# Kernel optimization log

Hardware: AMD Instinct MI355X
Metric: run time of the kernel (lower is better)

## Reference

```python
import jax, jax.numpy as jnp
import numpy as np

S, H, E, DFF = 8192, 1024, 8, 4096
CAPACITY = (S * 1) // E  # capacity_factor=1.0, k=1 -> 1024 (>= min_capacity 4)


def setup_inputs() -> dict:
    key = jax.random.key(0)
    ks = jax.random.split(key, 6)
    sc_in = 1.0 / np.sqrt(H)
    sc_ff = 1.0 / np.sqrt(DFF)
    return {
        "hidden_states": jax.random.normal(ks[0], (S, H), dtype=jnp.float32),
        "wg": jax.random.normal(ks[1], (H, E), dtype=jnp.float32) * sc_in,
        "w1": jax.random.normal(ks[2], (E, H, DFF), dtype=jnp.float32) * sc_in,
        "b1": jnp.zeros((E, DFF), dtype=jnp.float32),
        "w2": jax.random.normal(ks[3], (E, DFF, H), dtype=jnp.float32) * sc_ff,
        "b2": jnp.zeros((E, H), dtype=jnp.float32),
    }


def _top1_gate(x, wg):
    # DeepSpeed top1gating (noisy_gate_policy=None, used_token=None)
    logits = x @ wg                                   # [S, E]
    gates = jax.nn.softmax(logits, axis=-1)           # [S, E]
    idx = jnp.argmax(gates, axis=-1)                  # [S]
    mask1 = jax.nn.one_hot(idx, E, dtype=gates.dtype) # [S, E]
    # load-balancing aux loss (uses pre-capacity mask)
    me = jnp.mean(gates, axis=0)
    ce = jnp.mean(mask1, axis=0)
    l_aux = jnp.sum(me * ce) * E
    # capacity-based token dropping
    locations1 = jnp.cumsum(mask1, axis=0) - 1.0      # position within expert
    mask1 = mask1 * (locations1 < CAPACITY)
    exp_counts = jnp.sum(mask1, axis=0).astype(jnp.int32)
    loc_s = jnp.sum(locations1 * mask1, axis=1).astype(jnp.int32)   # [S]
    loc_sc = jax.nn.one_hot(loc_s, CAPACITY, dtype=gates.dtype)     # [S, C]
    combine = jnp.einsum("se,sc->sec", gates * mask1, loc_sc)       # [S, E, C]
    dispatch = (combine > 0).astype(gates.dtype)
    return l_aux, combine, dispatch, exp_counts


def reference(hidden_states, wg, w1, b1, w2, b2):
    l_aux, combine, dispatch, exp_counts = _top1_gate(hidden_states, wg)
    # dispatch tokens to expert slots: [E, C, H]
    disp = jnp.einsum("sec,sh->ech", dispatch, hidden_states)
    # grouped expert FFN (GELU MLP)
    h1 = jax.nn.gelu(jnp.einsum("ech,ehf->ecf", disp, w1) + b1[:, None, :])
    eo = jnp.einsum("ecf,efh->ech", h1, w2) + b2[:, None, :]
    # combine back to token order, weighted by gate values
    out = jnp.einsum("sec,ech->sh", combine, eo)      # [S, H]
    # dropout prob = 0.0 -> identity
    return out, l_aux, exp_counts
```

## Files before the change

### kernel.cpp

```cpp
#include <hip/hip_runtime.h>

#define S_TOK 8192
#define H_DIM 1024
#define NE    8
#define CAP   1024
#define DFF   4096

typedef unsigned short u16;
typedef __bf16 bf16_t;
typedef bf16_t bf16x8 __attribute__((ext_vector_type(8)));
typedef float  f32x4  __attribute__((ext_vector_type(4)));

__device__ __forceinline__ u16 f2bf(float f) {
  union { float f; unsigned u; } a; a.f = f;
  unsigned u = a.u;
  u += 0x7fffu + ((u >> 16) & 1u);
  return (u16)(u >> 16);
}

__device__ __forceinline__ float gelu_tanh(float x) {
  const float c = 0.7978845608028654f;
  float t = tanhf(c * (x + 0.044715f * x * x * x));
  return 0.5f * x * (1.0f + t);
}

__global__ void gate_kernel(const float* __restrict__ x, const float* __restrict__ wg,
                            float* __restrict__ gate, int* __restrict__ expert,
                            int* __restrict__ rank, int* __restrict__ blockCnt,
                            float* __restrict__ blockMe) {
  __shared__ float sg[16][8];
  __shared__ int   se[16];
  int tid = threadIdx.x, lane = tid & 63, w = tid >> 6;
  int b = blockIdx.x;
  for (int j = 0; j < 4; ++j) {
    int t = w * 4 + j;
    int s = b * 16 + t;
    const float* xr = x + (size_t)s * H_DIM;
    float acc[8];
#pragma unroll
    for (int e = 0; e < 8; ++e) acc[e] = 0.f;
#pragma unroll
    for (int i = 0; i < 16; ++i) {
      int h = i * 64 + lane;
      float xv = xr[h];
      float4 wa = *(const float4*)(wg + h * 8);
      float4 wb = *(const float4*)(wg + h * 8 + 4);
      acc[0] += xv * wa.x; acc[1] += xv * wa.y; acc[2] += xv * wa.z; acc[3] += xv * wa.w;
      acc[4] += xv * wb.x; acc[5] += xv * wb.y; acc[6] += xv * wb.z; acc[7] += xv * wb.w;
    }
#pragma unroll
    for (int off = 32; off >= 1; off >>= 1)
#pragma unroll
      for (int e = 0; e < 8; ++e) acc[e] += __shfl_down(acc[e], off);
    if (lane == 0) {
      float mx = acc[0];
#pragma unroll
      for (int e = 1; e < 8; ++e) mx = fmaxf(mx, acc[e]);
      float g[8], Z = 0.f;
#pragma unroll
      for (int e = 0; e < 8; ++e) { g[e] = expf(acc[e] - mx); Z += g[e]; }
      int am = 0; float best = acc[0];
#pragma unroll
      for (int e = 1; e < 8; ++e) if (acc[e] > best) { best = acc[e]; am = e; }
      float inv = 1.f / Z;
#pragma unroll
      for (int e = 0; e < 8; ++e) sg[t][e] = g[e] * inv;
      se[t] = am;
      gate[s] = g[am] * inv;
      expert[s] = am;
    }
  }
  __syncthreads();
  if (tid < 16) {
    int e = se[tid], r = 0;
    for (int t2 = 0; t2 < tid; ++t2) r += (se[t2] == e) ? 1 : 0;
    rank[b * 16 + tid] = r;
  }
  if (tid < 8) {
    int c = 0; float m = 0.f;
#pragma unroll
    for (int t = 0; t < 16; ++t) { c += (se[t] == tid) ? 1 : 0; m += sg[t][tid]; }
    blockCnt[b * 8 + tid] = c;
    blockMe[b * 8 + tid] = m;
  }
}

__global__ void scan_kernel(const int* __restrict__ blockCnt, const float* __restrict__ blockMe,
                            int* __restrict__ blockOff, int* __restrict__ counts,
                            float* __restrict__ tail) {
  int tid = threadIdx.x;
  int e = tid >> 6, lane = tid & 63;
  int run = 0; float msum = 0.f;
  for (int c = 0; c < 8; ++c) {
    int b = c * 64 + lane;
    int v = blockCnt[b * 8 + e];
    float mv = blockMe[b * 8 + e];
    int sc = v;
#pragma unroll
    for (int off = 1; off < 64; off <<= 1) {
      int u = __shfl_up(sc, off);
      if (lane >= off) sc += u;
    }
    blockOff[b * 8 + e] = run + sc - v;
    run += __shfl(sc, 63);
#pragma unroll
    for (int off = 32; off >= 1; off >>= 1) mv += __shfl_down(mv, off);
    msum += __shfl(mv, 0);
  }
  __shared__ float sm[8];
  __shared__ int scnt[8];
  if (lane == 0) {
    sm[e] = msum; scnt[e] = run;
    counts[e] = run < CAP ? run : CAP;
  }
  __syncthreads();
  if (tid == 0) {
    float la = 0.f;
    for (int i = 0; i < 8; ++i)
      la += (sm[i] / (float)S_TOK) * ((float)scnt[i] / (float)S_TOK);
    tail[0] = la * (float)NE;
    for (int i = 0; i < 8; ++i) {
      int cc = scnt[i] < CAP ? scnt[i] : CAP;
      tail[1 + i] = (float)cc;
    }
  }
}

__global__ void assign_kernel(const int* __restrict__ expert, const int* __restrict__ rank,
                              const int* __restrict__ blockOff, int* __restrict__ slot_token) {
  int s = blockIdx.x * 256 + threadIdx.x;
  int e = expert[s];
  int pos = blockOff[(s >> 4) * 8 + e] + rank[s];
  if (pos < CAP) slot_token[e * CAP + pos] = s;
}

__global__ void gather_kernel(const float* __restrict__ x, const int* __restrict__ slot_token,
                              const int* __restrict__ counts, u16* __restrict__ disp) {
  int slot = blockIdx.x;
  int e = slot >> 10, c = slot & 1023;
  int t = threadIdx.x;
  ushort4 v4;
  if (c < counts[e]) {
    int s = slot_token[slot];
    float4 v = *(const float4*)(x + (size_t)s * H_DIM + t * 4);
    v4.x = f2bf(v.x); v4.y = f2bf(v.y); v4.z = f2bf(v.z); v4.w = f2bf(v.w);
  } else {
    v4.x = 0; v4.y = 0; v4.z = 0; v4.w = 0;
  }
  *(ushort4*)(disp + (size_t)slot * H_DIM + t * 4) = v4;
}

__global__ void transpose_convert(const float* __restrict__ src0, u16* __restrict__ dst0,
                                  int R, int C) {
  __shared__ float tile[32][33];
  int e = blockIdx.z;
  const float* src = src0 + (size_t)e * R * C;
  u16* dst = dst0 + (size_t)e * R * C;
  int c0 = blockIdx.x * 32, r0 = blockIdx.y * 32;
  int xq = threadIdx.x & 31, yq = threadIdx.x >> 5;
#pragma unroll
  for (int i = 0; i < 32; i += 8)
    tile[yq + i][xq] = src[(size_t)(r0 + yq + i) * C + c0 + xq];
  __syncthreads();
#pragma unroll
  for (int i = 0; i < 32; i += 8)
    dst[(size_t)(c0 + yq + i) * R + r0 + xq] = f2bf(tile[xq][yq + i]);
}

__device__ __forceinline__ void stage_tile(const u16* g, int ldk, u16* lds) {
  int tid = threadIdx.x;
  int lane = tid & 63, w = tid >> 6;
#pragma unroll
  for (int r = 0; r < 2; ++r) {
    int p = (w * 2 + r) * 64 + lane;
    int row = p >> 2;
    int kq = (p & 3) ^ ((row >> 1) & 3);
    const u16* gp = g + (size_t)row * ldk + kq * 8;
    u16* lp = lds + (w * 2 + r) * 512;
    __builtin_amdgcn_global_load_lds((__attribute__((address_space(1))) int*)(gp),
                                     (__attribute__((address_space(3))) int*)(lp),
                                     16, 0, 0);
  }
}

template <int KDIM>
__device__ __forceinline__ void gemm_core(const u16* A, const u16* Bt, int lda, int ldb,
                                          u16* As, u16* Bs, f32x4 acc[4][4]) {
  int tid = threadIdx.x;
  int lane = tid & 63;
  int w = tid >> 6, wm = w >> 1, wn = w & 1;
  int q = lane >> 4, l15 = lane & 15;
  int aoff[4], boff[4];
#pragma unroll
  for (int t = 0; t < 4; ++t) {
    int ra = wm * 64 + t * 16 + l15;
    aoff[t] = ra * 32 + ((q ^ ((ra >> 1) & 3)) * 8);
    int rb = wn * 64 + t * 16 + l15;
    boff[t] = rb * 32 + ((q ^ ((rb >> 1) & 3)) * 8);
  }
  for (int kt = 0; kt < KDIM; kt += 32) {
    stage_tile(A + kt, lda, As);
    stage_tile(Bt + kt, ldb, Bs);
    __syncthreads();
    bf16x8 af[4], bfr[4];
#pragma unroll
    for (int t = 0; t < 4; ++t) af[t] = *(const bf16x8*)(As + aoff[t]);
#pragma unroll
    for (int t = 0; t < 4; ++t) bfr[t] = *(const bf16x8*)(Bs + boff[t]);
#pragma unroll
    for (int mt = 0; mt < 4; ++mt)
#pragma unroll
      for (int nt = 0; nt < 4; ++nt)
        acc[mt][nt] = __builtin_amdgcn_mfma_f32_16x16x32_bf16(af[mt], bfr[nt], acc[mt][nt], 0, 0, 0);
    __syncthreads();
  }
}

__global__ __launch_bounds__(256, 2) void gemm1_kernel(const u16* __restrict__ disp,
                                                       const u16* __restrict__ w1t,
                                                       const float* __restrict__ b1,
                                                       u16* __restrict__ h1) {
  __shared__ __align__(16) u16 As[4096];
  __shared__ __align__(16) u16 Bs[4096];
  int e = blockIdx.z;
  int m0 = blockIdx.y * 128, n0 = blockIdx.x * 128;
  const u16* A  = disp + (size_t)e * CAP * H_DIM + (size_t)m0 * H_DIM;
  const u16* Bt = w1t + (size_t)e * DFF * H_DIM + (size_t)n0 * H_DIM;
  f32x4 acc[4][4];
  f32x4 zero = {0.f, 0.f, 0.f, 0.f};
#pragma unroll
  for (int i = 0; i < 4; ++i)
#pragma unroll
    for (int j = 0; j < 4; ++j) acc[i][j] = zero;
  gemm_core<H_DIM>(A, Bt, H_DIM, H_DIM, As, Bs, acc);
  int tid = threadIdx.x, lane = tid & 63, w = tid >> 6, wm = w >> 1, wn = w & 1;
  int q = lane >> 4, l15 = lane & 15;
  const float* b1e = b1 + e * DFF;
  u16* out = h1 + (size_t)e * CAP * DFF;
#pragma unroll
  for (int mt = 0; mt < 4; ++mt)
#pragma unroll
    for (int nt = 0; nt < 4; ++nt) {
      int col = n0 + wn * 64 + nt * 16 + l15;
      float bias = b1e[col];
#pragma unroll
      for (int r = 0; r < 4; ++r) {
        int row = m0 + wm * 64 + mt * 16 + q * 4 + r;
        out[(size_t)row * DFF + col] = f2bf(gelu_tanh(acc[mt][nt][r] + bias));
      }
    }
}

__global__ __launch_bounds__(256, 2) void gemm2_kernel(const u16* __restrict__ h1,
                                                       const u16* __restrict__ w2t,
                                                       const float* __restrict__ b2,
                                                       const int* __restrict__ slot_token,
                                                       const float* __restrict__ gate,
                                                       const int* __restrict__ counts,
                                                       float* __restrict__ out) {
  __shared__ __align__(16) u16 As[4096];
  __shared__ __align__(16) u16 Bs[4096];
  int e = blockIdx.z;
  int m0 = blockIdx.y * 128, n0 = blockIdx.x * 128;
  const u16* A  = h1 + (size_t)e * CAP * DFF + (size_t)m0 * DFF;
  const u16* Bt = w2t + (size_t)e * H_DIM * DFF + (size_t)n0 * DFF;
  f32x4 acc[4][4];
  f32x4 zero = {0.f, 0.f, 0.f, 0.f};
#pragma unroll
  for (int i = 0; i < 4; ++i)
#pragma unroll
    for (int j = 0; j < 4; ++j) acc[i][j] = zero;
  gemm_core<DFF>(A, Bt, DFF, DFF, As, Bs, acc);
  int tid = threadIdx.x, lane = tid & 63, w = tid >> 6, wm = w >> 1, wn = w & 1;
  int q = lane >> 4, l15 = lane & 15;
  int cnt = counts[e];
  const float* b2e = b2 + e * H_DIM;
#pragma unroll
  for (int mt = 0; mt < 4; ++mt) {
    int tok[4]; float gv[4];
#pragma unroll
    for (int r = 0; r < 4; ++r) {
      int c = m0 + wm * 64 + mt * 16 + q * 4 + r;
      if (c < cnt) { int s = slot_token[e * CAP + c]; tok[r] = s; gv[r] = gate[s]; }
      else { tok[r] = -1; gv[r] = 0.f; }
    }
#pragma unroll
    for (int nt = 0; nt < 4; ++nt) {
      int col = n0 + wn * 64 + nt * 16 + l15;
      float bias = b2e[col];
#pragma unroll
      for (int r = 0; r < 4; ++r)
        if (tok[r] >= 0)
          out[(size_t)tok[r] * H_DIM + col] = gv[r] * (acc[mt][nt][r] + bias);
    }
  }
}

extern "C" void kernel_launch(void* const* d_in, const int* in_sizes, int n_in,
                              void* d_out, int out_size, void* d_ws, size_t ws_size,
                              hipStream_t stream) {
  const float* x  = (const float*)d_in[0];
  const float* wg = (const float*)d_in[1];
  const float* w1 = (const float*)d_in[2];
  const float* b1 = (const float*)d_in[3];
  const float* w2 = (const float*)d_in[4];
  const float* b2 = (const float*)d_in[5];
  float* out = (float*)d_out;
  char* ws = (char*)d_ws;
  const size_t MB = 1024 * 1024;
  u16* w1t  = (u16*)(ws);
  u16* w2t  = (u16*)(ws + 64 * MB);
  u16* disp = (u16*)(ws + 128 * MB);
  u16* h1   = (u16*)(ws + 144 * MB);
  char* sm = ws + 208 * MB;
  float* gate      = (float*)(sm);
  int*   expert    = (int*)(sm + 32 * 1024);
  int*   rank      = (int*)(sm + 64 * 1024);
  int*   slot_tok  = (int*)(sm + 96 * 1024);
  int*   blockCnt  = (int*)(sm + 128 * 1024);
  int*   blockOff  = (int*)(sm + 144 * 1024);
  float* blockMe   = (float*)(sm + 160 * 1024);
  int*   counts    = (int*)(sm + 176 * 1024);

  hipMemsetAsync(d_out, 0, (size_t)out_size * sizeof(float), stream);
  gate_kernel<<<512, 256, 0, stream>>>(x, wg, gate, expert, rank, blockCnt, blockMe);
  scan_kernel<<<1, 512, 0, stream>>>(blockCnt, blockMe, blockOff, counts,
                                     out + (size_t)S_TOK * H_DIM);
  assign_kernel<<<32, 256, 0, stream>>>(expert, rank, blockOff, slot_tok);
  gather_kernel<<<8192, 256, 0, stream>>>(x, slot_tok, counts, disp);
  transpose_convert<<<dim3(DFF / 32, H_DIM / 32, NE), 256, 0, stream>>>(w1, w1t, H_DIM, DFF);
  transpose_convert<<<dim3(H_DIM / 32, DFF / 32, NE), 256, 0, stream>>>(w2, w2t, DFF, H_DIM);
  gemm1_kernel<<<dim3(DFF / 128, CAP / 128, NE), 256, 0, stream>>>(disp, w1t, b1, h1);
  gemm2_kernel<<<dim3(H_DIM / 128, CAP / 128, NE), 256, 0, stream>>>(h1, w2t, b2,
                                                                     slot_tok, gate, counts, out);
}
```

Measured before the change: 631.0 us.

## Widen weight transpose to 64x64 vector tiles and give gemm2 eight waves

The weight transpose/convert kernel now works on 64x64 tiles with float4 loads and ushort4 bf16 stores instead of scalar 32x32 accesses, to cut memory transaction count. gemm2 now runs 512 threads per block with eight waves: half stage A and half stage B into LDS, and each wave computes a 64x32 sub-tile. This raises wave parallelism for the small 256-block grid. The new gemm2 inner loop is single-buffered with two barriers per k-step, so latency hiding rests on occupancy rather than prefetching.

```diff
diff --git a/kernel.cpp b/kernel.cpp
--- a/kernel.cpp
+++ b/kernel.cpp
@@ -152,19 +152,32 @@
 
 __global__ void transpose_convert(const float* __restrict__ src0, u16* __restrict__ dst0,
                                   int R, int C) {
-  __shared__ float tile[32][33];
+  __shared__ float tile[64][65];
   int e = blockIdx.z;
   const float* src = src0 + (size_t)e * R * C;
   u16* dst = dst0 + (size_t)e * R * C;
-  int c0 = blockIdx.x * 32, r0 = blockIdx.y * 32;
-  int xq = threadIdx.x & 31, yq = threadIdx.x >> 5;
-#pragma unroll
-  for (int i = 0; i < 32; i += 8)
-    tile[yq + i][xq] = src[(size_t)(r0 + yq + i) * C + c0 + xq];
+  int c0 = blockIdx.x * 64, r0 = blockIdx.y * 64;
+  int g = threadIdx.x & 15, rr = threadIdx.x >> 4;
+#pragma unroll
+  for (int p = 0; p < 4; ++p) {
+    int r = rr + p * 16;
+    float4 v = *(const float4*)(src + (size_t)(r0 + r) * C + c0 + g * 4);
+    tile[r][g * 4 + 0] = v.x;
+    tile[r][g * 4 + 1] = v.y;
+    tile[r][g * 4 + 2] = v.z;
+    tile[r][g * 4 + 3] = v.w;
+  }
   __syncthreads();
 #pragma unroll
-  for (int i = 0; i < 32; i += 8)
-    dst[(size_t)(c0 + yq + i) * R + r0 + xq] = f2bf(tile[xq][yq + i]);
+  for (int p = 0; p < 4; ++p) {
+    int c = rr + p * 16;
+    ushort4 o;
+    o.x = f2bf(tile[g * 4 + 0][c]);
+    o.y = f2bf(tile[g * 4 + 1][c]);
+    o.z = f2bf(tile[g * 4 + 2][c]);
+    o.w = f2bf(tile[g * 4 + 3][c]);
+    *(ushort4*)(dst + (size_t)(c0 + c) * R + r0 + g * 4) = o;
+  }
 }
 
 __device__ __forceinline__ void stage_tile(const u16* g, int ldk, u16* lds) {
@@ -251,7 +264,7 @@
     }
 }
 
-__global__ __launch_bounds__(256, 2) void gemm2_kernel(const u16* __restrict__ h1,
+__global__ __launch_bounds__(512, 4) void gemm2_kernel(const u16* __restrict__ h1,
                                                        const u16* __restrict__ w2t,
                                                        const float* __restrict__ b2,
                                                        const int* __restrict__ slot_token,
@@ -264,15 +277,59 @@
   int m0 = blockIdx.y * 128, n0 = blockIdx.x * 128;
   const u16* A  = h1 + (size_t)e * CAP * DFF + (size_t)m0 * DFF;
   const u16* Bt = w2t + (size_t)e * H_DIM * DFF + (size_t)n0 * DFF;
-  f32x4 acc[4][4];
+  int tid = threadIdx.x, lane = tid & 63, w = tid >> 6;
+  int wm = w >> 2, wn = w & 3;
+  int q = lane >> 4, l15 = lane & 15;
+  f32x4 acc[4][2];
   f32x4 zero = {0.f, 0.f, 0.f, 0.f};
 #pragma unroll
-  for (int i = 0; i < 4; ++i)
-#pragma unroll
-    for (int j = 0; j < 4; ++j) acc[i][j] = zero;
-  gemm_core<DFF>(A, Bt, DFF, DFF, As, Bs, acc);
-  int tid = threadIdx.x, lane = tid & 63, w = tid >> 6, wm = w >> 1, wn = w & 1;
-  int q = lane >> 4, l15 = lane & 15;
+  for (int i = 0; i < 4; ++i) { acc[i][0] = zero; acc[i][1] = zero; }
+
+  const u16* gsrc = (w < 4) ? A : Bt;
+  u16* ldst = (w < 4) ? As : Bs;
+  int q4 = w & 3;
+  const u16* gp0[2]; u16* lp[2];
+#pragma unroll
+  for (int r = 0; r < 2; ++r) {
+    int p = (q4 * 2 + r) * 64 + lane;
+    int srow = p >> 2;
+    int skq = (p & 3) ^ ((srow >> 1) & 3);
+    gp0[r] = gsrc + (size_t)srow * DFF + skq * 8;
+    lp[r] = ldst + (q4 * 2 + r) * 512;
+  }
+
+  int aoff[4], boff[2];
+#pragma unroll
+  for (int t = 0; t < 4; ++t) {
+    int ra = wm * 64 + t * 16 + l15;
+    aoff[t] = ra * 32 + ((q ^ ((ra >> 1) & 3)) * 8);
+  }
+#pragma unroll
+  for (int t = 0; t < 2; ++t) {
+    int rb = wn * 32 + t * 16 + l15;
+    boff[t] = rb * 32 + ((q ^ ((rb >> 1) & 3)) * 8);
+  }
+
+  for (int kt = 0; kt < DFF; kt += 32) {
+#pragma unroll
+    for (int r = 0; r < 2; ++r)
+      __builtin_amdgcn_global_load_lds((__attribute__((address_space(1))) int*)(gp0[r] + kt),
+                                       (__attribute__((address_space(3))) int*)(lp[r]),
+                                       16, 0, 0);
+    __syncthreads();
+    bf16x8 af[4], bfr[2];
+#pragma unroll
+    for (int t = 0; t < 4; ++t) af[t] = *(const bf16x8*)(As + aoff[t]);
+#pragma unroll
+    for (int t = 0; t < 2; ++t) bfr[t] = *(const bf16x8*)(Bs + boff[t]);
+#pragma unroll
+    for (int mt = 0; mt < 4; ++mt)
+#pragma unroll
+      for (int nt = 0; nt < 2; ++nt)
+        acc[mt][nt] = __builtin_amdgcn_mfma_f32_16x16x32_bf16(af[mt], bfr[nt], acc[mt][nt], 0, 0, 0);
+    __syncthreads();
+  }
+
   int cnt = counts[e];
   const float* b2e = b2 + e * H_DIM;
 #pragma unroll
@@ -285,8 +342,8 @@
       else { tok[r] = -1; gv[r] = 0.f; }
     }
 #pragma unroll
-    for (int nt = 0; nt < 4; ++nt) {
-      int col = n0 + wn * 64 + nt * 16 + l15;
+    for (int nt = 0; nt < 2; ++nt) {
+      int col = n0 + wn * 32 + nt * 16 + l15;
       float bias = b2e[col];
 #pragma unroll
       for (int r = 0; r < 4; ++r)
@@ -328,9 +385,9 @@
                                      out + (size_t)S_TOK * H_DIM);
   assign_kernel<<<32, 256, 0, stream>>>(expert, rank, blockOff, slot_tok);
   gather_kernel<<<8192, 256, 0, stream>>>(x, slot_tok, counts, disp);
-  transpose_convert<<<dim3(DFF / 32, H_DIM / 32, NE), 256, 0, stream>>>(w1, w1t, H_DIM, DFF);
-  transpose_convert<<<dim3(H_DIM / 32, DFF / 32, NE), 256, 0, stream>>>(w2, w2t, DFF, H_DIM);
+  transpose_convert<<<dim3(DFF / 64, H_DIM / 64, NE), 256, 0, stream>>>(w1, w1t, H_DIM, DFF);
+  transpose_convert<<<dim3(H_DIM / 64, DFF / 64, NE), 256, 0, stream>>>(w2, w2t, DFF, H_DIM);
   gemm1_kernel<<<dim3(DFF / 128, CAP / 128, NE), 256, 0, stream>>>(disp, w1t, b1, h1);
-  gemm2_kernel<<<dim3(H_DIM / 128, CAP / 128, NE), 256, 0, stream>>>(h1, w2t, b2,
+  gemm2_kernel<<<dim3(H_DIM / 128, CAP / 128, NE), 512, 0, stream>>>(h1, w2t, b2,
                                                                      slot_tok, gate, counts, out);
 }
```

Measured after the change: 616.5 us. 2.3% less time.

## Fuse fp32 weight conversion into GEMM B-tile staging and split-K gemm2

Applied to the files above, without the earlier changes.

Drops the two transpose_convert passes over the fp32 expert weights. Each GEMM now reads w1/w2 in fp32 directly, converts to bf16 in registers and writes a padded LDS tile. gemm2 is split into two K-halves that write fp32 partials, and a new combine kernel sums them, adds bias, applies the gate and scatters to token order. This removes a full read/write pass over about 256MB of weights and raises gemm2 parallelism. In exchange, every M-tile block re-reads and re-converts fp32 weights (8x redundant), B loads are no longer asynchronous LDS loads, and the partials add extra traffic.

```diff
diff --git a/kernel.cpp b/kernel.cpp
--- a/kernel.cpp
+++ b/kernel.cpp
@@ -10,6 +10,8 @@
 typedef __bf16 bf16_t;
 typedef bf16_t bf16x8 __attribute__((ext_vector_type(8)));
 typedef float  f32x4  __attribute__((ext_vector_type(4)));
+
+#define BSTRIDE 40
 
 __device__ __forceinline__ u16 f2bf(float f) {
   union { float f; unsigned u; } a; a.f = f;
@@ -150,57 +152,56 @@
   *(ushort4*)(disp + (size_t)slot * H_DIM + t * 4) = v4;
 }
 
-__global__ void transpose_convert(const float* __restrict__ src0, u16* __restrict__ dst0,
-                                  int R, int C) {
-  __shared__ float tile[32][33];
-  int e = blockIdx.z;
-  const float* src = src0 + (size_t)e * R * C;
-  u16* dst = dst0 + (size_t)e * R * C;
-  int c0 = blockIdx.x * 32, r0 = blockIdx.y * 32;
-  int xq = threadIdx.x & 31, yq = threadIdx.x >> 5;
-#pragma unroll
-  for (int i = 0; i < 32; i += 8)
-    tile[yq + i][xq] = src[(size_t)(r0 + yq + i) * C + c0 + xq];
-  __syncthreads();
-#pragma unroll
-  for (int i = 0; i < 32; i += 8)
-    dst[(size_t)(c0 + yq + i) * R + r0 + xq] = f2bf(tile[xq][yq + i]);
-}
-
-__device__ __forceinline__ void stage_tile(const u16* g, int ldk, u16* lds) {
+template <int NITER>
+__device__ __forceinline__ void gemm_fused(const u16* __restrict__ A, int lda,
+                                           const float* __restrict__ Bsrc, int ldn,
+                                           u16* As, u16* Bs, f32x4 acc[4][4]) {
   int tid = threadIdx.x;
-  int lane = tid & 63, w = tid >> 6;
+  int lane = tid & 63;
+  int w = tid >> 6, wm = w >> 1, wn = w & 1;
+  int q = lane >> 4, l15 = lane & 15;
+
+  const u16* agp[2]; u16* alp[2];
 #pragma unroll
   for (int r = 0; r < 2; ++r) {
     int p = (w * 2 + r) * 64 + lane;
     int row = p >> 2;
     int kq = (p & 3) ^ ((row >> 1) & 3);
-    const u16* gp = g + (size_t)row * ldk + kq * 8;
-    u16* lp = lds + (w * 2 + r) * 512;
-    __builtin_amdgcn_global_load_lds((__attribute__((address_space(1))) int*)(gp),
-                                     (__attribute__((address_space(3))) int*)(lp),
-                                     16, 0, 0);
-  }
-}
-
-template <int KDIM>
-__device__ __forceinline__ void gemm_core(const u16* A, const u16* Bt, int lda, int ldb,
-                                          u16* As, u16* Bs, f32x4 acc[4][4]) {
-  int tid = threadIdx.x;
-  int lane = tid & 63;
-  int w = tid >> 6, wm = w >> 1, wn = w & 1;
-  int q = lane >> 4, l15 = lane & 15;
+    agp[r] = A + (size_t)row * lda + kq * 8;
+    alp[r] = As + (w * 2 + r) * 512;
+  }
+
+  int nb = tid & 127, kh = tid >> 7;
+  const float* bbase = Bsrc + (size_t)(kh * 16) * ldn + nb;
+  u16* bdst = Bs + nb * BSTRIDE + kh * 16;
+
   int aoff[4], boff[4];
 #pragma unroll
   for (int t = 0; t < 4; ++t) {
     int ra = wm * 64 + t * 16 + l15;
     aoff[t] = ra * 32 + ((q ^ ((ra >> 1) & 3)) * 8);
     int rb = wn * 64 + t * 16 + l15;
-    boff[t] = rb * 32 + ((q ^ ((rb >> 1) & 3)) * 8);
-  }
-  for (int kt = 0; kt < KDIM; kt += 32) {
-    stage_tile(A + kt, lda, As);
-    stage_tile(Bt + kt, ldb, Bs);
+    boff[t] = rb * BSTRIDE + q * 8;
+  }
+
+  for (int kit = 0; kit < NITER; ++kit) {
+    int kt = kit * 32;
+#pragma unroll
+    for (int r = 0; r < 2; ++r)
+      __builtin_amdgcn_global_load_lds((__attribute__((address_space(1))) int*)(agp[r] + kt),
+                                       (__attribute__((address_space(3))) int*)(alp[r]),
+                                       16, 0, 0);
+    float v[16];
+    const float* bp = bbase + (size_t)kt * ldn;
+#pragma unroll
+    for (int i = 0; i < 16; ++i) v[i] = bp[(size_t)i * ldn];
+#pragma unroll
+    for (int p = 0; p < 4; ++p) {
+      unsigned lo = (unsigned)f2bf(v[p * 4 + 0]) | ((unsigned)f2bf(v[p * 4 + 1]) << 16);
+      unsigned hi = (unsigned)f2bf(v[p * 4 + 2]) | ((unsigned)f2bf(v[p * 4 + 3]) << 16);
+      uint2 pk; pk.x = lo; pk.y = hi;
+      *(uint2*)(bdst + p * 4) = pk;
+    }
     __syncthreads();
     bf16x8 af[4], bfr[4];
 #pragma unroll
@@ -217,22 +218,22 @@
 }
 
 __global__ __launch_bounds__(256, 2) void gemm1_kernel(const u16* __restrict__ disp,
-                                                       const u16* __restrict__ w1t,
+                                                       const float* __restrict__ w1,
                                                        const float* __restrict__ b1,
                                                        u16* __restrict__ h1) {
   __shared__ __align__(16) u16 As[4096];
-  __shared__ __align__(16) u16 Bs[4096];
+  __shared__ __align__(16) u16 Bs[128 * BSTRIDE];
   int e = blockIdx.z;
   int m0 = blockIdx.y * 128, n0 = blockIdx.x * 128;
-  const u16* A  = disp + (size_t)e * CAP * H_DIM + (size_t)m0 * H_DIM;
-  const u16* Bt = w1t + (size_t)e * DFF * H_DIM + (size_t)n0 * H_DIM;
+  const u16* A = disp + (size_t)e * CAP * H_DIM + (size_t)m0 * H_DIM;
+  const float* Bsrc = w1 + (size_t)e * H_DIM * DFF + n0;
   f32x4 acc[4][4];
   f32x4 zero = {0.f, 0.f, 0.f, 0.f};
 #pragma unroll
   for (int i = 0; i < 4; ++i)
 #pragma unroll
     for (int j = 0; j < 4; ++j) acc[i][j] = zero;
-  gemm_core<H_DIM>(A, Bt, H_DIM, H_DIM, As, Bs, acc);
+  gemm_fused<H_DIM / 32>(A, H_DIM, Bsrc, DFF, As, Bs, acc);
   int tid = threadIdx.x, lane = tid & 63, w = tid >> 6, wm = w >> 1, wn = w & 1;
   int q = lane >> 4, l15 = lane & 15;
   const float* b1e = b1 + e * DFF;
@@ -252,48 +253,59 @@
 }
 
 __global__ __launch_bounds__(256, 2) void gemm2_kernel(const u16* __restrict__ h1,
-                                                       const u16* __restrict__ w2t,
-                                                       const float* __restrict__ b2,
-                                                       const int* __restrict__ slot_token,
-                                                       const float* __restrict__ gate,
-                                                       const int* __restrict__ counts,
-                                                       float* __restrict__ out) {
+                                                       const float* __restrict__ w2,
+                                                       float* __restrict__ part) {
   __shared__ __align__(16) u16 As[4096];
-  __shared__ __align__(16) u16 Bs[4096];
-  int e = blockIdx.z;
+  __shared__ __align__(16) u16 Bs[128 * BSTRIDE];
+  int ez = blockIdx.z;
+  int e = ez >> 1, slice = ez & 1;
   int m0 = blockIdx.y * 128, n0 = blockIdx.x * 128;
-  const u16* A  = h1 + (size_t)e * CAP * DFF + (size_t)m0 * DFF;
-  const u16* Bt = w2t + (size_t)e * H_DIM * DFF + (size_t)n0 * DFF;
+  const u16* A = h1 + (size_t)e * CAP * DFF + (size_t)m0 * DFF + slice * 2048;
+  const float* Bsrc = w2 + (size_t)e * DFF * H_DIM + (size_t)(slice * 2048) * H_DIM + n0;
   f32x4 acc[4][4];
   f32x4 zero = {0.f, 0.f, 0.f, 0.f};
 #pragma unroll
   for (int i = 0; i < 4; ++i)
 #pragma unroll
     for (int j = 0; j < 4; ++j) acc[i][j] = zero;
-  gemm_core<DFF>(A, Bt, DFF, DFF, As, Bs, acc);
+  gemm_fused<2048 / 32>(A, DFF, Bsrc, H_DIM, As, Bs, acc);
   int tid = threadIdx.x, lane = tid & 63, w = tid >> 6, wm = w >> 1, wn = w & 1;
   int q = lane >> 4, l15 = lane & 15;
-  int cnt = counts[e];
-  const float* b2e = b2 + e * H_DIM;
-#pragma unroll
-  for (int mt = 0; mt < 4; ++mt) {
-    int tok[4]; float gv[4];
-#pragma unroll
-    for (int r = 0; r < 4; ++r) {
-      int c = m0 + wm * 64 + mt * 16 + q * 4 + r;
-      if (c < cnt) { int s = slot_token[e * CAP + c]; tok[r] = s; gv[r] = gate[s]; }
-      else { tok[r] = -1; gv[r] = 0.f; }
-    }
+  float* pout = part + ((size_t)(slice * 8 + e) * CAP) * H_DIM;
+#pragma unroll
+  for (int mt = 0; mt < 4; ++mt)
 #pragma unroll
     for (int nt = 0; nt < 4; ++nt) {
       int col = n0 + wn * 64 + nt * 16 + l15;
-      float bias = b2e[col];
-#pragma unroll
-      for (int r = 0; r < 4; ++r)
-        if (tok[r] >= 0)
-          out[(size_t)tok[r] * H_DIM + col] = gv[r] * (acc[mt][nt][r] + bias);
-    }
-  }
+#pragma unroll
+      for (int r = 0; r < 4; ++r) {
+        int row = m0 + wm * 64 + mt * 16 + q * 4 + r;
+        pout[(size_t)row * H_DIM + col] = acc[mt][nt][r];
+      }
+    }
+}
+
+__global__ void combine_kernel(const float* __restrict__ part, const float* __restrict__ b2,
+                               const int* __restrict__ slot_token,
+                               const float* __restrict__ gate,
+                               const int* __restrict__ counts, float* __restrict__ out) {
+  int slot = blockIdx.x;
+  int e = slot >> 10, c = slot & 1023;
+  if (c >= counts[e]) return;
+  int s = slot_token[slot];
+  float g = gate[s];
+  int t = threadIdx.x;
+  size_t base0 = ((size_t)e * CAP + c) * H_DIM + t * 4;
+  size_t base1 = ((size_t)(8 + e) * CAP + c) * H_DIM + t * 4;
+  float4 p0 = *(const float4*)(part + base0);
+  float4 p1 = *(const float4*)(part + base1);
+  float4 bb = *(const float4*)(b2 + e * H_DIM + t * 4);
+  float4 o;
+  o.x = g * (p0.x + p1.x + bb.x);
+  o.y = g * (p0.y + p1.y + bb.y);
+  o.z = g * (p0.z + p1.z + bb.z);
+  o.w = g * (p0.w + p1.w + bb.w);
+  *(float4*)(out + (size_t)s * H_DIM + t * 4) = o;
 }
 
 extern "C" void kernel_launch(void* const* d_in, const int* in_sizes, int n_in,
@@ -308,11 +320,10 @@
   float* out = (float*)d_out;
   char* ws = (char*)d_ws;
   const size_t MB = 1024 * 1024;
-  u16* w1t  = (u16*)(ws);
-  u16* w2t  = (u16*)(ws + 64 * MB);
-  u16* disp = (u16*)(ws + 128 * MB);
-  u16* h1   = (u16*)(ws + 144 * MB);
-  char* sm = ws + 208 * MB;
+  float* part = (float*)(ws);
+  u16* disp = (u16*)(ws + 64 * MB);
+  u16* h1   = (u16*)(ws + 80 * MB);
+  char* sm = ws + 144 * MB;
   float* gate      = (float*)(sm);
   int*   expert    = (int*)(sm + 32 * 1024);
   int*   rank      = (int*)(sm + 64 * 1024);
@@ -328,9 +339,7 @@
                                      out + (size_t)S_TOK * H_DIM);
   assign_kernel<<<32, 256, 0, stream>>>(expert, rank, blockOff, slot_tok);
   gather_kernel<<<8192, 256, 0, stream>>>(x, slot_tok, counts, disp);
-  transpose_convert<<<dim3(DFF / 32, H_DIM / 32, NE), 256, 0, stream>>>(w1, w1t, H_DIM, DFF);
-  transpose_convert<<<dim3(H_DIM / 32, DFF / 32, NE), 256, 0, stream>>>(w2, w2t, DFF, H_DIM);
-  gemm1_kernel<<<dim3(DFF / 128, CAP / 128, NE), 256, 0, stream>>>(disp, w1t, b1, h1);
-  gemm2_kernel<<<dim3(H_DIM / 128, CAP / 128, NE), 256, 0, stream>>>(h1, w2t, b2,
-                                                                     slot_tok, gate, counts, out);
-}
+  gemm1_kernel<<<dim3(DFF / 128, CAP / 128, NE), 256, 0, stream>>>(disp, w1, b1, h1);
+  gemm2_kernel<<<dim3(H_DIM / 128, CAP / 128, NE * 2), 256, 0, stream>>>(h1, w2, part);
+  combine_kernel<<<NE * CAP, 256, 0, stream>>>(part, b2, slot_tok, gate, counts, out);
+}
```

After: 647.8 us. +2.7%, slower.
